# Kernel tuning notes

Hardware: AMD Instinct MI355X
Metric: run time of the kernel (lower is better)

The kernel has to match this reference:

```python
import jax, jax.numpy as jnp
import numpy as np

B, S, DIM, HEADS, DEPTH = 8, 8192, 128, 8, 4


def setup_inputs() -> dict:
    key = jax.random.key(0)
    k1, k2, k3, k4 = jax.random.split(key, 4)
    x = jax.random.normal(k1, (B, S, DIM), dtype=jnp.float32)
    # nn.Parameter(torch.randn(depth, heads, dim, dim))
    weights = jax.random.normal(k2, (DEPTH, HEADS, DIM, DIM), dtype=jnp.float32)
    # nn.Linear(dim*heads, dim): stored here as [in, out] for x @ w_mix + b_mix
    bound = 1.0 / np.sqrt(DIM * HEADS)
    w_mix = jax.random.uniform(k3, (DIM * HEADS, DIM), dtype=jnp.float32,
                               minval=-bound, maxval=bound)
    b_mix = jax.random.uniform(k4, (DIM,), dtype=jnp.float32,
                               minval=-bound, maxval=bound)
    return {"x": x, "weights": weights, "w_mix": w_mix, "b_mix": b_mix}


def fractal_forward(x, weights, w_mix, b_mix):
    # Recursive binary tree over the sequence axis, collapsed into per-level
    # vectorized passes: level k (k = 1..depth) processes 2^(depth-k) segments
    # of length S / 2^(depth-k) with shared weights[k-1].
    b, s, d = x.shape
    depth, heads = weights.shape[0], weights.shape[1]
    for k in range(1, depth + 1):
        n = 2 ** (depth - k)          # number of tree segments at this level
        L = s // n                    # segment length
        x4 = x.reshape(b, n, L, d)
        # per-head matmul: stack over heads first (matches torch.stack order)
        mh = jnp.einsum('bnld,hde->bnhle', x4, weights[k - 1])  # [B,n,H,L,D]
        # faithful to .transpose(0,1).contiguous().view(B, L, H*D):
        # row-major reinterpretation of [H, L, D] as [L, H*D] per segment
        flat = mh.reshape(b, n, L, heads * d)
        y = flat @ w_mix + b_mix      # head_mixing Linear -> [B,n,L,D]
        x = y.reshape(b, s, d)
    return x


def reference(x, weights, w_mix, b_mix):
    return fractal_forward(x, weights, w_mix, b_mix)
```

## Files before the change

### kernel.cpp

```cpp
#include <hip/hip_runtime.h>
#include <hip/hip_bf16.h>


typedef __attribute__((ext_vector_type(8))) __bf16 bf16x8;
typedef __attribute__((ext_vector_type(8))) _Float16 half8;
typedef __attribute__((ext_vector_type(4))) float f32x4;
typedef __attribute__((ext_vector_type(4))) unsigned short us4;
typedef __attribute__((ext_vector_type(8))) unsigned short us8;

#define DEVI static __device__ __forceinline__

DEVI unsigned short f2bf(float f) {
  unsigned u = __builtin_bit_cast(unsigned, f);
  unsigned r = (u + 0x7fffu + ((u >> 16) & 1u)) >> 16;
  return (unsigned short)r;
}
DEVI float bf2f(unsigned short s) {
  return __builtin_bit_cast(float, (unsigned)s << 16);
}
DEVI unsigned short f2h(float f) {
  return __builtin_bit_cast(unsigned short, (_Float16)f);
}

DEVI void gload_lds16(const void* g, void* l) {
  __builtin_amdgcn_global_load_lds(
      (const __attribute__((address_space(1))) void*)g,
      (__attribute__((address_space(3))) void*)l,
      16, 0, 0);
}

__global__ __launch_bounds__(256) void split_kernel(
    const float* __restrict__ x, unsigned short* __restrict__ hi,
    unsigned short* __restrict__ lo, int n4)
{
  const int stride = gridDim.x * 256;
  for (int i = blockIdx.x * 256 + threadIdx.x; i < n4; i += stride) {
    const float4 v = ((const float4*)x)[i];
    float vv[4] = {v.x, v.y, v.z, v.w};
    us4 hv, lv;
#pragma unroll
    for (int t = 0; t < 4; ++t) {
      const unsigned short hb = f2bf(vv[t]);
      hv[t] = hb;
      lv[t] = f2bf(vv[t] - bf2f(hb));
    }
    ((us4*)hi)[i] = hv;
    ((us4*)lo)[i] = lv;
  }
}

__global__ __launch_bounds__(256) void split_f16(
    const float* __restrict__ x, unsigned short* __restrict__ o, int n4)
{
  const int stride = gridDim.x * 256;
  for (int i = blockIdx.x * 256 + threadIdx.x; i < n4; i += stride) {
    const float4 v = ((const float4*)x)[i];
    us4 hv;
    hv[0] = f2h(v.x);
    hv[1] = f2h(v.y);
    hv[2] = f2h(v.z);
    hv[3] = f2h(v.w);
    ((us4*)o)[i] = hv;
  }
}

__global__ __launch_bounds__(256) void wmixT_split(
    const float* __restrict__ wmix, unsigned short* __restrict__ Th,
    unsigned short* __restrict__ Tl)
{
  __shared__ float sT[128][129];
  const int j = blockIdx.x;
  const int tid = threadIdx.x;
  const float* src = wmix + (size_t)j * 16384;
  for (int i = tid; i < 16384 / 4; i += 256) {
    const int d2 = i >> 5;
    const int e4 = (i & 31) * 4;
    const float4 v = *(const float4*)(src + d2 * 128 + e4);
    sT[e4 + 0][d2] = v.x;
    sT[e4 + 1][d2] = v.y;
    sT[e4 + 2][d2] = v.z;
    sT[e4 + 3][d2] = v.w;
  }
  __syncthreads();
  const int e = tid >> 1;
  const int d2h = (tid & 1) * 64;
  const size_t base = (size_t)e * 1024 + j * 128 + d2h;
#pragma unroll
  for (int r = 0; r < 8; ++r) {
    us8 hv, lv;
#pragma unroll
    for (int t = 0; t < 8; ++t) {
      const float m = sT[e][d2h + r * 8 + t];
      const unsigned short hb = f2bf(m);
      hv[t] = hb;
      lv[t] = f2bf(m - bf2f(hb));
    }
    *(us8*)(Th + base + r * 8) = hv;
    *(us8*)(Tl + base + r * 8) = lv;
  }
}

__global__ __launch_bounds__(256, 2) void precompute_MT_mfma(
    const unsigned short* __restrict__ Ah, const unsigned short* __restrict__ Al,
    const unsigned short* __restrict__ Bh, const unsigned short* __restrict__ Bl,
    unsigned short* __restrict__ MT16)
{
  __shared__ unsigned short sAh[128 * 64];
  __shared__ unsigned short sAl[128 * 64];
  __shared__ unsigned short sBh[128 * 64];
  __shared__ unsigned short sBl[128 * 64];

  const int tid = threadIdx.x;
  const int j = blockIdx.x;
  const int lvlh = blockIdx.y;

  const int w = tid >> 6, lane = tid & 63;
  const int srow = w * 8 + (lane >> 3);
  const int scol = (lane & 7) * 8;
  const size_t aoff = (size_t)srow * 1024 + j * 128 + scol;
  const size_t boff = (size_t)lvlh * 16384 + (size_t)srow * 128 + scol;
  const int ldst = w * 512;

  f32x4 acc[4][4] = {};
  const int wm = w >> 1, wn = w & 1;

  for (int kb = 0; kb < 2; ++kb) {
    const int kc = kb * 64;
#pragma unroll
    for (int i = 0; i < 4; ++i) {
      const int lo_ = ldst + i * 2048;
      gload_lds16(Ah + aoff + (size_t)i * 32 * 1024 + kc, sAh + lo_);
      gload_lds16(Al + aoff + (size_t)i * 32 * 1024 + kc, sAl + lo_);
      gload_lds16(Bh + boff + (size_t)i * 32 * 128 + kc, sBh + lo_);
      gload_lds16(Bl + boff + (size_t)i * 32 * 128 + kc, sBl + lo_);
    }
    __syncthreads();
#pragma unroll
    for (int kk = 0; kk < 2; ++kk) {
      bf16x8 fah[4], fal[4], fbh[4], fbl[4];
      const int ko = kk * 32 + ((lane >> 4) << 3);
#pragma unroll
      for (int m = 0; m < 4; ++m) {
        const int row = wm * 64 + m * 16 + (lane & 15);
        fah[m] = *(const bf16x8*)(sAh + row * 64 + ko);
        fal[m] = *(const bf16x8*)(sAl + row * 64 + ko);
      }
#pragma unroll
      for (int n = 0; n < 4; ++n) {
        const int col = wn * 64 + n * 16 + (lane & 15);
        fbh[n] = *(const bf16x8*)(sBh + col * 64 + ko);
        fbl[n] = *(const bf16x8*)(sBl + col * 64 + ko);
      }
#pragma unroll
      for (int m = 0; m < 4; ++m) {
#pragma unroll
        for (int n = 0; n < 4; ++n) {
          acc[m][n] = __builtin_amdgcn_mfma_f32_16x16x32_bf16(
              fah[m], fbh[n], acc[m][n], 0, 0, 0);
          acc[m][n] = __builtin_amdgcn_mfma_f32_16x16x32_bf16(
              fah[m], fbl[n], acc[m][n], 0, 0, 0);
          acc[m][n] = __builtin_amdgcn_mfma_f32_16x16x32_bf16(
              fal[m], fbh[n], acc[m][n], 0, 0, 0);
        }
      }
    }
    __syncthreads();
  }

  const size_t mtbase = (size_t)lvlh * 131072 + (size_t)j * 128;
#pragma unroll
  for (int m = 0; m < 4; ++m) {
#pragma unroll
    for (int n = 0; n < 4; ++n) {
      const int d = wn * 64 + n * 16 + (lane & 15);
#pragma unroll
      for (int i = 0; i < 4; ++i) {
        const int e = wm * 64 + m * 16 + ((lane >> 4) << 2) + i;
        MT16[mtbase + (size_t)e * 1024 + d] = f2h(acc[m][n][i]);
      }
    }
  }
}

template <int OUT_MODE>
__global__ __launch_bounds__(256, 2) void level_gemm_f16(
    const unsigned short* __restrict__ A, const unsigned short* __restrict__ B,
    const float* __restrict__ bias, unsigned short* __restrict__ O16,
    float* __restrict__ Ofp, int lshift)
{
  __shared__ unsigned short sA[2][128 * 64];
  __shared__ unsigned short sB[2][128 * 64];

  const int tid = threadIdx.x;
  const int h = blockIdx.y;
  const int g0 = blockIdx.x * 128;

  const int w = tid >> 6, lane = tid & 63;
  const int srow = w * 8 + (lane >> 3);
  const int xcol = ((lane & 7) ^ (lane >> 3)) * 8;
  const size_t aoff = (size_t)(g0 + srow) * 1024 + xcol;
  const size_t boff = (size_t)(h * 128 + srow) * 1024 + xcol;
  const int ldst = w * 512;

  f32x4 acc[4][4] = {};
  const int wm = w >> 1, wn = w & 1;

#define STAGE_LG(buf, kc_)                                                  \
  {                                                                         \
    _Pragma("unroll") for (int i_ = 0; i_ < 4; ++i_) {                      \
      const size_t go_ = (size_t)i_ * 32 * 1024 + (size_t)(kc_);            \
      const int lo_ = ldst + i_ * 2048;                                     \
      gload_lds16(A + aoff + go_, sA[buf] + lo_);                           \
      gload_lds16(B + boff + go_, sB[buf] + lo_);                           \
    }                                                                       \
  }

  STAGE_LG(0, 0);
  int cur = 0;
  for (int kb = 0; kb < 16; ++kb) {
    if (kb < 15) {
      STAGE_LG(cur ^ 1, (kb + 1) * 64);
      asm volatile("s_waitcnt vmcnt(8)" ::: "memory");
    } else {
      asm volatile("s_waitcnt vmcnt(0)" ::: "memory");
    }
    __builtin_amdgcn_sched_barrier(0);
    __builtin_amdgcn_s_barrier();
    __builtin_amdgcn_sched_barrier(0);
    const unsigned short* sAc = sA[cur];
    const unsigned short* sBc = sB[cur];
#pragma unroll
    for (int kk = 0; kk < 2; ++kk) {
      half8 fa[4], fb[4];
      const int ko = (kk * 32 + ((lane >> 4) << 3)) ^ ((lane & 7) << 3);
#pragma unroll
      for (int m = 0; m < 4; ++m) {
        const int row = wm * 64 + m * 16 + (lane & 15);
        fa[m] = *(const half8*)(sAc + row * 64 + ko);
      }
#pragma unroll
      for (int n = 0; n < 4; ++n) {
        const int col = wn * 64 + n * 16 + (lane & 15);
        fb[n] = *(const half8*)(sBc + col * 64 + ko);
      }
#pragma unroll
      for (int m = 0; m < 4; ++m) {
#pragma unroll
        for (int n = 0; n < 4; ++n) {
          acc[m][n] = __builtin_amdgcn_mfma_f32_16x16x32_f16(
              fa[m], fb[n], acc[m][n], 0, 0, 0);
        }
      }
    }
    __builtin_amdgcn_sched_barrier(0);
    __builtin_amdgcn_s_barrier();
    __builtin_amdgcn_sched_barrier(0);
    cur ^= 1;
  }
#undef STAGE_LG

  const int bss = lshift - 3;
  const int q = g0 & 1023;
  const int n_idx = q >> bss;
  const int r0 = q & ((1 << bss) - 1);
  const long srow0 = (long)(g0 >> 10) * 8192 + ((long)n_idx << lshift) +
                     ((long)h << bss) + r0;
  const size_t obase = (size_t)srow0 * 128;

#pragma unroll
  for (int m = 0; m < 4; ++m) {
#pragma unroll
    for (int n = 0; n < 4; ++n) {
      const int col = wn * 64 + n * 16 + (lane & 15);
      const float bv = bias[col];
#pragma unroll
      for (int i = 0; i < 4; ++i) {
        const int row = wm * 64 + m * 16 + ((lane >> 4) << 2) + i;
        const float v = acc[m][n][i] + bv;
        const size_t p = obase + (size_t)row * 128 + col;
        if (OUT_MODE) {
          Ofp[p] = v;
        } else {
          O16[p] = f2h(v);
        }
      }
    }
  }
}

extern "C" void kernel_launch(void* const* d_in, const int* in_sizes, int n_in,
                              void* d_out, int out_size, void* d_ws,
                              size_t ws_size, hipStream_t stream) {
  const float* x = (const float*)d_in[0];
  const float* W = (const float*)d_in[1];
  const float* wmx = (const float*)d_in[2];
  const float* bmx = (const float*)d_in[3];
  float* out = (float*)d_out;

  const size_t NELEM = 8ull * 8192 * 128;
  const size_t MTSZ = 4ull * 1024 * 1024;
  const size_t WSZ = 4ull * 8 * 128 * 128;
  const size_t WTSZ = 128ull * 1024;

  unsigned short* MT16 = (unsigned short*)d_ws;
  unsigned short* Wh = MT16 + MTSZ;
  unsigned short* Wl = Wh + WSZ;
  unsigned short* wTh = Wl + WSZ;
  unsigned short* wTl = wTh + WTSZ;
  unsigned short* Xa = wTl + WTSZ;
  unsigned short* Xc = Xa + NELEM;
  unsigned short* Xb = (unsigned short*)d_out;

  split_kernel<<<dim3(512), dim3(256), 0, stream>>>(W, Wh, Wl, (int)(WSZ / 4));
  wmixT_split<<<dim3(8), dim3(256), 0, stream>>>(wmx, wTh, wTl);
  precompute_MT_mfma<<<dim3(8, 32), dim3(256), 0, stream>>>(wTh, wTl, Wh, Wl,
                                                            MT16);
  split_f16<<<dim3(2048), dim3(256), 0, stream>>>(x, Xa, (int)(NELEM / 4));

  dim3 grid(64, 8), blk(256);
  level_gemm_f16<0><<<grid, blk, 0, stream>>>(Xa, MT16 + 0 * 1048576ull, bmx,
                                              Xb, nullptr, 10);
  level_gemm_f16<0><<<grid, blk, 0, stream>>>(Xb, MT16 + 1 * 1048576ull, bmx,
                                              Xc, nullptr, 11);
  level_gemm_f16<0><<<grid, blk, 0, stream>>>(Xc, MT16 + 2 * 1048576ull, bmx,
                                              Xa, nullptr, 12);
  level_gemm_f16<1><<<grid, blk, 0, stream>>>(Xa, MT16 + 3 * 1048576ull, bmx,
                                              nullptr, out, 13);
}
```

Before: 119.1 us.

## Halve K-tile in level GEMM to double occupancy, add MFMA priority

The level GEMM now stages 32-wide K chunks instead of 64, halving LDS use per block. This allows launch bounds of 4 blocks per CU instead of 2, and the loop runs 32 iterations with a new XOR swizzle and fewer loads per stage. s_setprio is raised around the MFMA block so matrix work gets issue priority. The trade-off is twice as many barriers per tile and register pressure under the tighter launch bound, which could cause spills.

```diff
diff --git a/kernel.cpp b/kernel.cpp
--- a/kernel.cpp
+++ b/kernel.cpp
@@ -183,44 +183,46 @@
 }
 
 template <int OUT_MODE>
-__global__ __launch_bounds__(256, 2) void level_gemm_f16(
+__global__ __launch_bounds__(256, 4) void level_gemm_f16(
     const unsigned short* __restrict__ A, const unsigned short* __restrict__ B,
     const float* __restrict__ bias, unsigned short* __restrict__ O16,
     float* __restrict__ Ofp, int lshift)
 {
-  __shared__ unsigned short sA[2][128 * 64];
-  __shared__ unsigned short sB[2][128 * 64];
+  __shared__ unsigned short sA[2][128 * 32];
+  __shared__ unsigned short sB[2][128 * 32];
 
   const int tid = threadIdx.x;
   const int h = blockIdx.y;
   const int g0 = blockIdx.x * 128;
 
   const int w = tid >> 6, lane = tid & 63;
-  const int srow = w * 8 + (lane >> 3);
-  const int xcol = ((lane & 7) ^ (lane >> 3)) * 8;
-  const size_t aoff = (size_t)(g0 + srow) * 1024 + xcol;
-  const size_t boff = (size_t)(h * 128 + srow) * 1024 + xcol;
-  const int ldst = w * 512;
+  const int srow = tid >> 2;
+  const int xslot = (tid & 3) ^ (srow & 3);
+  const size_t aoff = (size_t)(g0 + srow) * 1024 + xslot * 8;
+  const size_t boff = (size_t)(h * 128 + srow) * 1024 + xslot * 8;
+  const int ldsw = w * 512;
 
   f32x4 acc[4][4] = {};
   const int wm = w >> 1, wn = w & 1;
 
 #define STAGE_LG(buf, kc_)                                                  \
   {                                                                         \
-    _Pragma("unroll") for (int i_ = 0; i_ < 4; ++i_) {                      \
-      const size_t go_ = (size_t)i_ * 32 * 1024 + (size_t)(kc_);            \
-      const int lo_ = ldst + i_ * 2048;                                     \
-      gload_lds16(A + aoff + go_, sA[buf] + lo_);                           \
-      gload_lds16(B + boff + go_, sB[buf] + lo_);                           \
-    }                                                                       \
+    gload_lds16(A + aoff + (size_t)(kc_), sA[buf] + ldsw);                  \
+    gload_lds16(A + aoff + 65536 + (size_t)(kc_), sA[buf] + 2048 + ldsw);   \
+    gload_lds16(B + boff + (size_t)(kc_), sB[buf] + ldsw);                  \
+    gload_lds16(B + boff + 65536 + (size_t)(kc_), sB[buf] + 2048 + ldsw);   \
   }
 
   STAGE_LG(0, 0);
   int cur = 0;
-  for (int kb = 0; kb < 16; ++kb) {
-    if (kb < 15) {
-      STAGE_LG(cur ^ 1, (kb + 1) * 64);
-      asm volatile("s_waitcnt vmcnt(8)" ::: "memory");
+  const int l15 = lane & 15;
+  const int ko = ((lane >> 4) ^ (lane & 3)) << 3;
+
+#pragma unroll 1
+  for (int kb = 0; kb < 32; ++kb) {
+    if (kb < 31) {
+      STAGE_LG(cur ^ 1, (kb + 1) * 32);
+      asm volatile("s_waitcnt vmcnt(4)" ::: "memory");
     } else {
       asm volatile("s_waitcnt vmcnt(0)" ::: "memory");
     }
@@ -229,29 +231,27 @@
     __builtin_amdgcn_sched_barrier(0);
     const unsigned short* sAc = sA[cur];
     const unsigned short* sBc = sB[cur];
-#pragma unroll
-    for (int kk = 0; kk < 2; ++kk) {
-      half8 fa[4], fb[4];
-      const int ko = (kk * 32 + ((lane >> 4) << 3)) ^ ((lane & 7) << 3);
-#pragma unroll
-      for (int m = 0; m < 4; ++m) {
-        const int row = wm * 64 + m * 16 + (lane & 15);
-        fa[m] = *(const half8*)(sAc + row * 64 + ko);
-      }
+    half8 fa[4], fb[4];
+#pragma unroll
+    for (int m = 0; m < 4; ++m) {
+      const int row = wm * 64 + m * 16 + l15;
+      fa[m] = *(const half8*)(sAc + row * 32 + ko);
+    }
+#pragma unroll
+    for (int n = 0; n < 4; ++n) {
+      const int col = wn * 64 + n * 16 + l15;
+      fb[n] = *(const half8*)(sBc + col * 32 + ko);
+    }
+    __builtin_amdgcn_s_setprio(1);
+#pragma unroll
+    for (int m = 0; m < 4; ++m) {
 #pragma unroll
       for (int n = 0; n < 4; ++n) {
-        const int col = wn * 64 + n * 16 + (lane & 15);
-        fb[n] = *(const half8*)(sBc + col * 64 + ko);
-      }
-#pragma unroll
-      for (int m = 0; m < 4; ++m) {
-#pragma unroll
-        for (int n = 0; n < 4; ++n) {
-          acc[m][n] = __builtin_amdgcn_mfma_f32_16x16x32_f16(
-              fa[m], fb[n], acc[m][n], 0, 0, 0);
-        }
-      }
-    }
+        acc[m][n] = __builtin_amdgcn_mfma_f32_16x16x32_f16(
+            fa[m], fb[n], acc[m][n], 0, 0, 0);
+      }
+    }
+    __builtin_amdgcn_s_setprio(0);
     __builtin_amdgcn_sched_barrier(0);
     __builtin_amdgcn_s_barrier();
     __builtin_amdgcn_sched_barrier(0);
@@ -271,7 +271,7 @@
   for (int m = 0; m < 4; ++m) {
 #pragma unroll
     for (int n = 0; n < 4; ++n) {
-      const int col = wn * 64 + n * 16 + (lane & 15);
+      const int col = wn * 64 + n * 16 + l15;
       const float bv = bias[col];
 #pragma unroll
       for (int i = 0; i < 4; ++i) {
```

Measured after the change: 136.7 us. 1.15x slower.

## Fuse weight prep into one kernel and fold x fp16 cast into first GEMM

Applied to the files above, without the earlier changes.

Four small preprocessing kernels (weight bf16 hi/lo split, w_mix transpose-split, MT precompute, x fp16 conversion) are replaced by one fused_prep kernel and an fp32-input mode of the first level GEMM. That mode loads fp32 x, converts it to fp16 in registers and writes it to LDS. The aim is to save launches and the full round trip of x through an fp16 buffer in memory. Costs: the first GEMM reads twice the bytes and does conversion on its critical path, fused_prep does strided global reads with a single block per CU, and s_setprio is added around the MFMA loops.

```diff
diff --git a/kernel.cpp b/kernel.cpp
--- a/kernel.cpp
+++ b/kernel.cpp
@@ -5,7 +5,6 @@
 typedef __attribute__((ext_vector_type(8))) __bf16 bf16x8;
 typedef __attribute__((ext_vector_type(8))) _Float16 half8;
 typedef __attribute__((ext_vector_type(4))) float f32x4;
-typedef __attribute__((ext_vector_type(4))) unsigned short us4;
 typedef __attribute__((ext_vector_type(8))) unsigned short us8;
 
 #define DEVI static __device__ __forceinline__
@@ -29,127 +28,77 @@
       16, 0, 0);
 }
 
-__global__ __launch_bounds__(256) void split_kernel(
-    const float* __restrict__ x, unsigned short* __restrict__ hi,
-    unsigned short* __restrict__ lo, int n4)
-{
-  const int stride = gridDim.x * 256;
-  for (int i = blockIdx.x * 256 + threadIdx.x; i < n4; i += stride) {
-    const float4 v = ((const float4*)x)[i];
-    float vv[4] = {v.x, v.y, v.z, v.w};
-    us4 hv, lv;
-#pragma unroll
-    for (int t = 0; t < 4; ++t) {
-      const unsigned short hb = f2bf(vv[t]);
-      hv[t] = hb;
-      lv[t] = f2bf(vv[t] - bf2f(hb));
-    }
-    ((us4*)hi)[i] = hv;
-    ((us4*)lo)[i] = lv;
-  }
-}
-
-__global__ __launch_bounds__(256) void split_f16(
-    const float* __restrict__ x, unsigned short* __restrict__ o, int n4)
-{
-  const int stride = gridDim.x * 256;
-  for (int i = blockIdx.x * 256 + threadIdx.x; i < n4; i += stride) {
-    const float4 v = ((const float4*)x)[i];
-    us4 hv;
-    hv[0] = f2h(v.x);
-    hv[1] = f2h(v.y);
-    hv[2] = f2h(v.z);
-    hv[3] = f2h(v.w);
-    ((us4*)o)[i] = hv;
-  }
-}
-
-__global__ __launch_bounds__(256) void wmixT_split(
-    const float* __restrict__ wmix, unsigned short* __restrict__ Th,
-    unsigned short* __restrict__ Tl)
-{
-  __shared__ float sT[128][129];
-  const int j = blockIdx.x;
-  const int tid = threadIdx.x;
-  const float* src = wmix + (size_t)j * 16384;
-  for (int i = tid; i < 16384 / 4; i += 256) {
-    const int d2 = i >> 5;
-    const int e4 = (i & 31) * 4;
-    const float4 v = *(const float4*)(src + d2 * 128 + e4);
-    sT[e4 + 0][d2] = v.x;
-    sT[e4 + 1][d2] = v.y;
-    sT[e4 + 2][d2] = v.z;
-    sT[e4 + 3][d2] = v.w;
-  }
-  __syncthreads();
-  const int e = tid >> 1;
-  const int d2h = (tid & 1) * 64;
-  const size_t base = (size_t)e * 1024 + j * 128 + d2h;
-#pragma unroll
-  for (int r = 0; r < 8; ++r) {
-    us8 hv, lv;
-#pragma unroll
-    for (int t = 0; t < 8; ++t) {
-      const float m = sT[e][d2h + r * 8 + t];
-      const unsigned short hb = f2bf(m);
-      hv[t] = hb;
-      lv[t] = f2bf(m - bf2f(hb));
-    }
-    *(us8*)(Th + base + r * 8) = hv;
-    *(us8*)(Tl + base + r * 8) = lv;
-  }
-}
-
-__global__ __launch_bounds__(256, 2) void precompute_MT_mfma(
-    const unsigned short* __restrict__ Ah, const unsigned short* __restrict__ Al,
-    const unsigned short* __restrict__ Bh, const unsigned short* __restrict__ Bl,
+__global__ __launch_bounds__(256, 1) void fused_prep(
+    const float* __restrict__ W, const float* __restrict__ wmix,
     unsigned short* __restrict__ MT16)
 {
-  __shared__ unsigned short sAh[128 * 64];
-  __shared__ unsigned short sAl[128 * 64];
-  __shared__ unsigned short sBh[128 * 64];
-  __shared__ unsigned short sBl[128 * 64];
-
-  const int tid = threadIdx.x;
+  __shared__ unsigned short sAh[128 * 136];
+  __shared__ unsigned short sAl[128 * 136];
+  __shared__ unsigned short sBh[128 * 136];
+  __shared__ unsigned short sBl[128 * 136];
+
   const int j = blockIdx.x;
   const int lvlh = blockIdx.y;
+  const int tid = threadIdx.x;
+
+  {
+    const int d = tid >> 1, c0 = (tid & 1) * 64;
+    const float* srcW = W + (size_t)lvlh * 16384 + (size_t)d * 128 + c0;
+#pragma unroll
+    for (int r8 = 0; r8 < 64; r8 += 8) {
+      us8 hv, lv;
+#pragma unroll
+      for (int t = 0; t < 8; ++t) {
+        const float m = srcW[r8 + t];
+        const unsigned short hb = f2bf(m);
+        hv[t] = hb;
+        lv[t] = f2bf(m - bf2f(hb));
+      }
+      *(us8*)(sBh + d * 136 + c0 + r8) = hv;
+      *(us8*)(sBl + d * 136 + c0 + r8) = lv;
+    }
+  }
+  {
+    const int e = tid >> 1, c0 = (tid & 1) * 64;
+    const float* srcM = wmix + (size_t)(j * 128 + c0) * 128 + e;
+#pragma unroll
+    for (int r8 = 0; r8 < 64; r8 += 8) {
+      us8 hv, lv;
+#pragma unroll
+      for (int t = 0; t < 8; ++t) {
+        const float m = srcM[(size_t)(r8 + t) * 128];
+        const unsigned short hb = f2bf(m);
+        hv[t] = hb;
+        lv[t] = f2bf(m - bf2f(hb));
+      }
+      *(us8*)(sAh + e * 136 + c0 + r8) = hv;
+      *(us8*)(sAl + e * 136 + c0 + r8) = lv;
+    }
+  }
+  __syncthreads();
 
   const int w = tid >> 6, lane = tid & 63;
-  const int srow = w * 8 + (lane >> 3);
-  const int scol = (lane & 7) * 8;
-  const size_t aoff = (size_t)srow * 1024 + j * 128 + scol;
-  const size_t boff = (size_t)lvlh * 16384 + (size_t)srow * 128 + scol;
-  const int ldst = w * 512;
-
+  const int wm = w >> 1, wn = w & 1;
+  const int l15 = lane & 15;
   f32x4 acc[4][4] = {};
-  const int wm = w >> 1, wn = w & 1;
-
+
+#pragma unroll
   for (int kb = 0; kb < 2; ++kb) {
-    const int kc = kb * 64;
-#pragma unroll
-    for (int i = 0; i < 4; ++i) {
-      const int lo_ = ldst + i * 2048;
-      gload_lds16(Ah + aoff + (size_t)i * 32 * 1024 + kc, sAh + lo_);
-      gload_lds16(Al + aoff + (size_t)i * 32 * 1024 + kc, sAl + lo_);
-      gload_lds16(Bh + boff + (size_t)i * 32 * 128 + kc, sBh + lo_);
-      gload_lds16(Bl + boff + (size_t)i * 32 * 128 + kc, sBl + lo_);
-    }
-    __syncthreads();
 #pragma unroll
     for (int kk = 0; kk < 2; ++kk) {
+      const int ko = kb * 64 + kk * 32 + ((lane >> 4) << 3);
       bf16x8 fah[4], fal[4], fbh[4], fbl[4];
-      const int ko = kk * 32 + ((lane >> 4) << 3);
 #pragma unroll
       for (int m = 0; m < 4; ++m) {
-        const int row = wm * 64 + m * 16 + (lane & 15);
-        fah[m] = *(const bf16x8*)(sAh + row * 64 + ko);
-        fal[m] = *(const bf16x8*)(sAl + row * 64 + ko);
+        const int row = wm * 64 + m * 16 + l15;
+        fah[m] = *(const bf16x8*)(sAh + row * 136 + ko);
+        fal[m] = *(const bf16x8*)(sAl + row * 136 + ko);
       }
 #pragma unroll
       for (int n = 0; n < 4; ++n) {
-        const int col = wn * 64 + n * 16 + (lane & 15);
-        fbh[n] = *(const bf16x8*)(sBh + col * 64 + ko);
-        fbl[n] = *(const bf16x8*)(sBl + col * 64 + ko);
+        const int col = wn * 64 + n * 16 + l15;
+        fbh[n] = *(const bf16x8*)(sBh + col * 136 + ko);
+        fbl[n] = *(const bf16x8*)(sBl + col * 136 + ko);
       }
 #pragma unroll
       for (int m = 0; m < 4; ++m) {
@@ -164,7 +113,6 @@
         }
       }
     }
-    __syncthreads();
   }
 
   const size_t mtbase = (size_t)lvlh * 131072 + (size_t)j * 128;
@@ -172,7 +120,7 @@
   for (int m = 0; m < 4; ++m) {
 #pragma unroll
     for (int n = 0; n < 4; ++n) {
-      const int d = wn * 64 + n * 16 + (lane & 15);
+      const int d = wn * 64 + n * 16 + l15;
 #pragma unroll
       for (int i = 0; i < 4; ++i) {
         const int e = wm * 64 + m * 16 + ((lane >> 4) << 2) + i;
@@ -182,11 +130,11 @@
   }
 }
 
-template <int OUT_MODE>
+template <int IN_MODE, int OUT_MODE>
 __global__ __launch_bounds__(256, 2) void level_gemm_f16(
-    const unsigned short* __restrict__ A, const unsigned short* __restrict__ B,
-    const float* __restrict__ bias, unsigned short* __restrict__ O16,
-    float* __restrict__ Ofp, int lshift)
+    const float* __restrict__ A32, const unsigned short* __restrict__ A16,
+    const unsigned short* __restrict__ B, const float* __restrict__ bias,
+    unsigned short* __restrict__ O16, float* __restrict__ Ofp, int lshift)
 {
   __shared__ unsigned short sA[2][128 * 64];
   __shared__ unsigned short sB[2][128 * 64];
@@ -204,60 +152,117 @@
 
   f32x4 acc[4][4] = {};
   const int wm = w >> 1, wn = w & 1;
-
+  const int l15 = lane & 15;
+
+#define COMPUTE_TILE(sAc, sBc)                                              \
+  {                                                                         \
+    _Pragma("unroll") for (int kk = 0; kk < 2; ++kk) {                      \
+      half8 fa[4], fb[4];                                                   \
+      const int ko = (kk * 32 + ((lane >> 4) << 3)) ^ ((lane & 7) << 3);    \
+      _Pragma("unroll") for (int m = 0; m < 4; ++m) {                       \
+        fa[m] = *(const half8*)((sAc) + (wm * 64 + m * 16 + l15) * 64 + ko);\
+      }                                                                     \
+      _Pragma("unroll") for (int n = 0; n < 4; ++n) {                       \
+        fb[n] = *(const half8*)((sBc) + (wn * 64 + n * 16 + l15) * 64 + ko);\
+      }                                                                     \
+      __builtin_amdgcn_s_setprio(1);                                        \
+      _Pragma("unroll") for (int m = 0; m < 4; ++m) {                       \
+        _Pragma("unroll") for (int n = 0; n < 4; ++n) {                     \
+          acc[m][n] = __builtin_amdgcn_mfma_f32_16x16x32_f16(               \
+              fa[m], fb[n], acc[m][n], 0, 0, 0);                            \
+        }                                                                   \
+      }                                                                     \
+      __builtin_amdgcn_s_setprio(0);                                        \
+    }                                                                       \
+  }
+
+#define SFENCE() __builtin_amdgcn_sched_barrier(0)
+
+  if constexpr (IN_MODE == 0) {
 #define STAGE_LG(buf, kc_)                                                  \
-  {                                                                         \
-    _Pragma("unroll") for (int i_ = 0; i_ < 4; ++i_) {                      \
-      const size_t go_ = (size_t)i_ * 32 * 1024 + (size_t)(kc_);            \
-      const int lo_ = ldst + i_ * 2048;                                     \
-      gload_lds16(A + aoff + go_, sA[buf] + lo_);                           \
-      gload_lds16(B + boff + go_, sB[buf] + lo_);                           \
-    }                                                                       \
-  }
-
-  STAGE_LG(0, 0);
-  int cur = 0;
-  for (int kb = 0; kb < 16; ++kb) {
-    if (kb < 15) {
-      STAGE_LG(cur ^ 1, (kb + 1) * 64);
-      asm volatile("s_waitcnt vmcnt(8)" ::: "memory");
-    } else {
-      asm volatile("s_waitcnt vmcnt(0)" ::: "memory");
-    }
-    __builtin_amdgcn_sched_barrier(0);
-    __builtin_amdgcn_s_barrier();
-    __builtin_amdgcn_sched_barrier(0);
-    const unsigned short* sAc = sA[cur];
-    const unsigned short* sBc = sB[cur];
-#pragma unroll
-    for (int kk = 0; kk < 2; ++kk) {
-      half8 fa[4], fb[4];
-      const int ko = (kk * 32 + ((lane >> 4) << 3)) ^ ((lane & 7) << 3);
-#pragma unroll
-      for (int m = 0; m < 4; ++m) {
-        const int row = wm * 64 + m * 16 + (lane & 15);
-        fa[m] = *(const half8*)(sAc + row * 64 + ko);
-      }
-#pragma unroll
-      for (int n = 0; n < 4; ++n) {
-        const int col = wn * 64 + n * 16 + (lane & 15);
-        fb[n] = *(const half8*)(sBc + col * 64 + ko);
-      }
-#pragma unroll
-      for (int m = 0; m < 4; ++m) {
-#pragma unroll
-        for (int n = 0; n < 4; ++n) {
-          acc[m][n] = __builtin_amdgcn_mfma_f32_16x16x32_f16(
-              fa[m], fb[n], acc[m][n], 0, 0, 0);
-        }
-      }
-    }
-    __builtin_amdgcn_sched_barrier(0);
-    __builtin_amdgcn_s_barrier();
-    __builtin_amdgcn_sched_barrier(0);
-    cur ^= 1;
-  }
+    {                                                                       \
+      _Pragma("unroll") for (int i_ = 0; i_ < 4; ++i_) {                    \
+        const size_t go_ = (size_t)i_ * 32 * 1024 + (size_t)(kc_);          \
+        const int lo_ = ldst + i_ * 2048;                                   \
+        gload_lds16(A16 + aoff + go_, sA[buf] + lo_);                       \
+        gload_lds16(B + boff + go_, sB[buf] + lo_);                         \
+      }                                                                     \
+    }
+    STAGE_LG(0, 0);
+    int cur = 0;
+#pragma unroll 1
+    for (int kb = 0; kb < 16; ++kb) {
+      if (kb < 15) {
+        STAGE_LG(cur ^ 1, (kb + 1) * 64);
+        asm volatile("s_waitcnt vmcnt(8)" ::: "memory");
+      } else {
+        asm volatile("s_waitcnt vmcnt(0)" ::: "memory");
+      }
+      SFENCE();
+      __builtin_amdgcn_s_barrier();
+      SFENCE();
+      COMPUTE_TILE(sA[cur], sB[cur]);
+      SFENCE();
+      __builtin_amdgcn_s_barrier();
+      SFENCE();
+      cur ^= 1;
+    }
 #undef STAGE_LG
+  } else {
+    float4 av0[4], av1[4];
+#define ISS_A(kc_)                                                          \
+    {                                                                       \
+      _Pragma("unroll") for (int i_ = 0; i_ < 4; ++i_) {                    \
+        const float* p_ = A32 + aoff + (size_t)i_ * 32768 + (size_t)(kc_);  \
+        av0[i_] = *(const float4*)p_;                                       \
+        av1[i_] = *(const float4*)(p_ + 4);                                 \
+      }                                                                     \
+    }
+#define WR_A(buf)                                                           \
+    {                                                                       \
+      _Pragma("unroll") for (int i_ = 0; i_ < 4; ++i_) {                    \
+        us8 hv_;                                                            \
+        hv_[0] = f2h(av0[i_].x); hv_[1] = f2h(av0[i_].y);                   \
+        hv_[2] = f2h(av0[i_].z); hv_[3] = f2h(av0[i_].w);                   \
+        hv_[4] = f2h(av1[i_].x); hv_[5] = f2h(av1[i_].y);                   \
+        hv_[6] = f2h(av1[i_].z); hv_[7] = f2h(av1[i_].w);                   \
+        *(us8*)(sA[buf] + ldst + i_ * 2048 + lane * 8) = hv_;               \
+      }                                                                     \
+    }
+#define STG_B(buf, kc_)                                                     \
+    {                                                                       \
+      _Pragma("unroll") for (int i_ = 0; i_ < 4; ++i_) {                    \
+        gload_lds16(B + boff + (size_t)i_ * 32768 + (size_t)(kc_),          \
+                    sB[buf] + ldst + i_ * 2048);                            \
+      }                                                                     \
+    }
+    ISS_A(0);
+    STG_B(0, 0);
+#pragma unroll 1
+    for (int kb = 0; kb < 16; ++kb) {
+      const int cur = kb & 1;
+      asm volatile("s_waitcnt vmcnt(4)" ::: "memory");
+      WR_A(cur);
+      asm volatile("s_waitcnt vmcnt(0) lgkmcnt(0)" ::: "memory");
+      SFENCE();
+      __builtin_amdgcn_s_barrier();
+      SFENCE();
+      if (kb < 15) {
+        ISS_A((kb + 1) * 64);
+        STG_B(cur ^ 1, (kb + 1) * 64);
+      }
+      SFENCE();
+      COMPUTE_TILE(sA[cur], sB[cur]);
+      SFENCE();
+      __builtin_amdgcn_s_barrier();
+      SFENCE();
+    }
+#undef ISS_A
+#undef WR_A
+#undef STG_B
+  }
+#undef COMPUTE_TILE
+#undef SFENCE
 
   const int bss = lshift - 3;
   const int q = g0 & 1023;
@@ -271,7 +276,7 @@
   for (int m = 0; m < 4; ++m) {
 #pragma unroll
     for (int n = 0; n < 4; ++n) {
-      const int col = wn * 64 + n * 16 + (lane & 15);
+      const int col = wn * 64 + n * 16 + l15;
       const float bv = bias[col];
 #pragma unroll
       for (int i = 0; i < 4; ++i) {
@@ -299,31 +304,21 @@
 
   const size_t NELEM = 8ull * 8192 * 128;
   const size_t MTSZ = 4ull * 1024 * 1024;
-  const size_t WSZ = 4ull * 8 * 128 * 128;
-  const size_t WTSZ = 128ull * 1024;
 
   unsigned short* MT16 = (unsigned short*)d_ws;
-  unsigned short* Wh = MT16 + MTSZ;
-  unsigned short* Wl = Wh + WSZ;
-  unsigned short* wTh = Wl + WSZ;
-  unsigned short* wTl = wTh + WTSZ;
-  unsigned short* Xa = wTl + WTSZ;
+  unsigned short* Xa = MT16 + MTSZ;
   unsigned short* Xc = Xa + NELEM;
   unsigned short* Xb = (unsigned short*)d_out;
 
-  split_kernel<<<dim3(512), dim3(256), 0, stream>>>(W, Wh, Wl, (int)(WSZ / 4));
-  wmixT_split<<<dim3(8), dim3(256), 0, stream>>>(wmx, wTh, wTl);
-  precompute_MT_mfma<<<dim3(8, 32), dim3(256), 0, stream>>>(wTh, wTl, Wh, Wl,
-                                                            MT16);
-  split_f16<<<dim3(2048), dim3(256), 0, stream>>>(x, Xa, (int)(NELEM / 4));
+  fused_prep<<<dim3(8, 32), dim3(256), 0, stream>>>(W, wmx, MT16);
 
   dim3 grid(64, 8), blk(256);
-  level_gemm_f16<0><<<grid, blk, 0, stream>>>(Xa, MT16 + 0 * 1048576ull, bmx,
-                                              Xb, nullptr, 10);
-  level_gemm_f16<0><<<grid, blk, 0, stream>>>(Xb, MT16 + 1 * 1048576ull, bmx,
-                                              Xc, nullptr, 11);
-  level_gemm_f16<0><<<grid, blk, 0, stream>>>(Xc, MT16 + 2 * 1048576ull, bmx,
-                                              Xa, nullptr, 12);
-  level_gemm_f16<1><<<grid, blk, 0, stream>>>(Xa, MT16 + 3 * 1048576ull, bmx,
-                                              nullptr, out, 13);
-}
+  level_gemm_f16<1, 0><<<grid, blk, 0, stream>>>(
+      x, nullptr, MT16 + 0 * 1048576ull, bmx, Xb, nullptr, 10);
+  level_gemm_f16<0, 0><<<grid, blk, 0, stream>>>(
+      nullptr, Xb, MT16 + 1 * 1048576ull, bmx, Xc, nullptr, 11);
+  level_gemm_f16<0, 0><<<grid, blk, 0, stream>>>(
+      nullptr, Xc, MT16 + 2 * 1048576ull, bmx, Xa, nullptr, 12);
+  level_gemm_f16<0, 1><<<grid, blk, 0, stream>>>(
+      nullptr, Xa, MT16 + 3 * 1048576ull, bmx, nullptr, out, 13);
+}
```

After: 108.2 us (median of 2 runs). 9.1% less time.
